# Performance work log

Measured on AMD Instinct MI355X. Metric: run time of the kernel, lower is better.

Reference implementation:

```python
import jax, jax.numpy as jnp
import numpy as np

BATCH = 4096
NUM_FEATURES = 2048
DEPTH = 4
KERNEL = 2
THRESHOLD = 0.0


def setup_inputs() -> dict:
    key = jax.random.key(0)
    keys = jax.random.split(key, 2 + 2 * DEPTH + 2)
    inp = {}
    inp['x'] = jax.random.normal(keys[0], (BATCH, NUM_FEATURES), dtype=jnp.float32)
    # Conv2d(1,1,kernel_size=2) weight (k,k) and scalar bias, PyTorch-style init scale
    fan_in = KERNEL * KERNEL
    bound = 1.0 / np.sqrt(fan_in)
    inp['conv_w'] = jax.random.uniform(keys[1], (KERNEL, KERNEL), jnp.float32, -bound, bound)
    inp['conv_b'] = jax.random.uniform(keys[2], (), jnp.float32, -bound, bound)
    # MLP hidden layers
    lb = 1.0 / np.sqrt(NUM_FEATURES)
    for i in range(DEPTH):
        inp[f'W{i}'] = jax.random.uniform(keys[3 + 2 * i], (NUM_FEATURES, NUM_FEATURES), jnp.float32, -lb, lb)
        inp[f'b{i}'] = jax.random.uniform(keys[4 + 2 * i], (NUM_FEATURES,), jnp.float32, -lb, lb)
    inp['Wh'] = jax.random.uniform(keys[3 + 2 * DEPTH], (2, NUM_FEATURES), jnp.float32, -lb, lb)
    inp['bh'] = jax.random.uniform(keys[4 + 2 * DEPTH], (2,), jnp.float32, -lb, lb)
    return inp


def reference(x, conv_w, conv_b, W0, b0, W1, b1, W2, b2, W3, b3, Wh, bh):
    # Per-feature ConvFilter on a constant k x k patch of value x_i collapses to
    # sigmoid(x_i * sum(conv_w) + conv_b - threshold)  -- one fused elementwise op.
    h = jax.nn.sigmoid(x * jnp.sum(conv_w) + conv_b - THRESHOLD)  # (B, F)
    for W, b in ((W0, b0), (W1, b1), (W2, b2), (W3, b3)):
        h = jax.nn.relu(h @ W.T + b)
    return h @ Wh.T + bh  # (B, 2)
```

## Files before the change

kernel.cpp:

```cpp
#include <hip/hip_runtime.h>
#include <math.h>

#define BATCH 4096
#define NF    2048

typedef signed char    i8;
typedef unsigned int   u32;
typedef __attribute__((ext_vector_type(4))) int   intx4;
typedef __attribute__((ext_vector_type(4))) float floatx4;

#define LBW 0.022097086912079612f
#define QMAX 32512.0f
#define AMAX_H 3.0f

__global__ __launch_bounds__(256) void prep_kernel(
    const float* __restrict__ x, const float* __restrict__ cw,
    const float* __restrict__ cb,
    const float* __restrict__ w0, const float* __restrict__ w1,
    const float* __restrict__ w2, const float* __restrict__ w3,
    i8* __restrict__ h1o, i8* __restrict__ h2o,
    i8* __restrict__ q1,  i8* __restrict__ q2)
{
    const int bid = blockIdx.x;
    if (bid < 8192) {
        const float s = cw[0] + cw[1] + cw[2] + cw[3];
        const float c = cb[0];
        const int i = bid * 256 + threadIdx.x;
        float4 v = ((const float4*)x)[i];
        float vv[4] = {v.x, v.y, v.z, v.w};
        char4 c1, c2;
        #pragma unroll
        for (int j = 0; j < 4; ++j) {
            float r = 1.0f / (1.0f + expf(-(vv[j] * s + c)));
            int X = (int)(r * QMAX + 0.5f);
            int h1 = (X + 128) >> 8;
            int h2 = X - (h1 << 8);
            ((i8*)&c1)[j] = (i8)h1;
            ((i8*)&c2)[j] = (i8)h2;
        }
        *(char4*)&h1o[(size_t)i * 4] = c1;
        *(char4*)&h2o[(size_t)i * 4] = c2;
    } else {
        const int b2    = bid - 8192;
        const int layer = b2 >> 12;
        const int i     = (b2 & 4095) * 256 + threadIdx.x;
        const float* w = (layer == 0) ? w0 : (layer == 1) ? w1
                       : (layer == 2) ? w2 : w3;
        const size_t base = (size_t)layer * (size_t)NF * NF;
        float4 v = ((const float4*)w)[i];
        float vv[4] = {v.x, v.y, v.z, v.w};
        char4 c1, c2;
        #pragma unroll
        for (int j = 0; j < 4; ++j) {
            int X = (int)floorf(vv[j] * (QMAX / LBW) + 0.5f);
            X = max(-32512, min(32512, X));
            int h1 = (X + 128) >> 8;
            int h2 = X - (h1 << 8);
            ((i8*)&c1)[j] = (i8)h1;
            ((i8*)&c2)[j] = (i8)h2;
        }
        *(char4*)&q1[base + (size_t)i * 4] = c1;
        *(char4*)&q2[base + (size_t)i * 4] = c2;
    }
}

#define BM 256
#define BN 128
#define BK 64

#define BUFSZ  49152
#define SEC_A1 0
#define SEC_A2 16384
#define SEC_B1 32768
#define SEC_B2 40960

__device__ __forceinline__ void stage16(const void* g, void* l) {
    __builtin_amdgcn_global_load_lds(
        (const __attribute__((address_space(1))) u32*)g,
        (__attribute__((address_space(3))) u32*)l, 16, 0, 0);
}

__global__ __launch_bounds__(512, 2) void gemm_i8_split(
    const i8* __restrict__ A1, const i8* __restrict__ A2,
    const i8* __restrict__ B1, const i8* __restrict__ B2,
    const float* __restrict__ bias,
    i8* __restrict__ C1, i8* __restrict__ C2,
    const float* __restrict__ Wh, const float* __restrict__ bh,
    float* __restrict__ outp,
    float combo, float outscale, int last, int M, int N, int K)
{
    extern __shared__ i8 smem[];

    const int t    = threadIdx.x;
    const int wv   = t >> 6;
    const int ln   = t & 63;
    const int quad = ln >> 4;
    const int ml   = ln & 15;
    const int wm   = wv >> 1;
    const int wn   = wv & 1;
    const int bm   = blockIdx.y * BM;
    const int bn   = blockIdx.x * BN;
    const int lnoff = ln * 16;

    int rA0 = (bm + (wv * 2 + 0) * 16 + ml) * K + quad * 16;
    int rA1 = (bm + (wv * 2 + 1) * 16 + ml) * K + quad * 16;
    int rB  = (bn +  wv * 16          + ml) * K + quad * 16;

    intx4 zero = {0, 0, 0, 0};
    intx4 acc11[4][4], accX[4][4];
    #pragma unroll
    for (int i = 0; i < 4; ++i)
        #pragma unroll
        for (int j = 0; j < 4; ++j) { acc11[i][j] = zero; accX[i][j] = zero; }

    stage16(A1 + rA0, smem + 0 * BUFSZ + SEC_A1 + (wv * 2 + 0) * 1024);
    stage16(A1 + rA1, smem + 0 * BUFSZ + SEC_A1 + (wv * 2 + 1) * 1024);
    stage16(A2 + rA0, smem + 0 * BUFSZ + SEC_A2 + (wv * 2 + 0) * 1024);
    stage16(A2 + rA1, smem + 0 * BUFSZ + SEC_A2 + (wv * 2 + 1) * 1024);
    stage16(B1 + rB,  smem + 0 * BUFSZ + SEC_B1 + wv * 1024);
    stage16(B2 + rB,  smem + 0 * BUFSZ + SEC_B2 + wv * 1024);
    rA0 += BK; rA1 += BK; rB += BK;
    stage16(A1 + rA0, smem + 1 * BUFSZ + SEC_A1 + (wv * 2 + 0) * 1024);
    stage16(A1 + rA1, smem + 1 * BUFSZ + SEC_A1 + (wv * 2 + 1) * 1024);
    stage16(A2 + rA0, smem + 1 * BUFSZ + SEC_A2 + (wv * 2 + 0) * 1024);
    stage16(A2 + rA1, smem + 1 * BUFSZ + SEC_A2 + (wv * 2 + 1) * 1024);
    stage16(B1 + rB,  smem + 1 * BUFSZ + SEC_B1 + wv * 1024);
    stage16(B2 + rB,  smem + 1 * BUFSZ + SEC_B2 + wv * 1024);
    rA0 += BK; rA1 += BK; rB += BK;
    asm volatile("s_waitcnt vmcnt(6)" ::: "memory");
    __builtin_amdgcn_s_barrier();
    asm volatile("" ::: "memory");

    int rdbase = 0;
    int wrbase = 2 * BUFSZ;

    intx4 a1f0, a1f1, a2f0, a2f1;
    intx4 b1lo0, b1lo1, b2lo0, b2lo1, b1hi0, b1hi1, b2hi0, b2hi1;

#define LDA_(SEC, c) (*(const intx4*)&smem[rdbase + (SEC) + (c) * 1024 + lnoff])
#define MFMA3(i, j, A1R, A2R, B1R, B2R) \
    acc11[i][j] = __builtin_amdgcn_mfma_i32_16x16x64_i8(A1R, B1R, acc11[i][j], 0, 0, 0); \
    accX [i][j] = __builtin_amdgcn_mfma_i32_16x16x64_i8(A1R, B2R, accX [i][j], 0, 0, 0); \
    accX [i][j] = __builtin_amdgcn_mfma_i32_16x16x64_i8(A2R, B1R, accX [i][j], 0, 0, 0);
#define FENCE_   asm volatile("" ::: "memory")
#define BARRIER_ FENCE_; __builtin_amdgcn_s_barrier(); FENCE_
#define LGKM0_   asm volatile("s_waitcnt lgkmcnt(0)" ::: "memory")

    const int NIT = K >> 6;
    #pragma unroll 1
    for (int kt = 0; kt < NIT; ++kt) {
        const int sg = (kt < NIT - 2);
        a1f0 = LDA_(SEC_A1, wm * 4 + 0);  a1f1 = LDA_(SEC_A1, wm * 4 + 1);
        a2f0 = LDA_(SEC_A2, wm * 4 + 0);  a2f1 = LDA_(SEC_A2, wm * 4 + 1);
        b1lo0 = LDA_(SEC_B1, wn * 4 + 0); b1lo1 = LDA_(SEC_B1, wn * 4 + 1);
        b2lo0 = LDA_(SEC_B2, wn * 4 + 0); b2lo1 = LDA_(SEC_B2, wn * 4 + 1);
        if (sg) {
            stage16(A1 + rA0, smem + wrbase + SEC_A1 + (wv * 2 + 0) * 1024);
            stage16(A1 + rA1, smem + wrbase + SEC_A1 + (wv * 2 + 1) * 1024);
            stage16(A2 + rA0, smem + wrbase + SEC_A2 + (wv * 2 + 0) * 1024);
            stage16(A2 + rA1, smem + wrbase + SEC_A2 + (wv * 2 + 1) * 1024);
        }
        BARRIER_; LGKM0_;
        __builtin_amdgcn_s_setprio(1);
        MFMA3(0, 0, a1f0, a2f0, b1lo0, b2lo0) MFMA3(0, 1, a1f0, a2f0, b1lo1, b2lo1)
        MFMA3(1, 0, a1f1, a2f1, b1lo0, b2lo0) MFMA3(1, 1, a1f1, a2f1, b1lo1, b2lo1)
        __builtin_amdgcn_s_setprio(0);
        BARRIER_;
        b1hi0 = LDA_(SEC_B1, wn * 4 + 2); b1hi1 = LDA_(SEC_B1, wn * 4 + 3);
        b2hi0 = LDA_(SEC_B2, wn * 4 + 2); b2hi1 = LDA_(SEC_B2, wn * 4 + 3);
        if (sg) {
            stage16(B1 + rB, smem + wrbase + SEC_B1 + wv * 1024);
            stage16(B2 + rB, smem + wrbase + SEC_B2 + wv * 1024);
            rA0 += BK; rA1 += BK; rB += BK;
        }
        BARRIER_; LGKM0_;
        __builtin_amdgcn_s_setprio(1);
        MFMA3(0, 2, a1f0, a2f0, b1hi0, b2hi0) MFMA3(0, 3, a1f0, a2f0, b1hi1, b2hi1)
        MFMA3(1, 2, a1f1, a2f1, b1hi0, b2hi0) MFMA3(1, 3, a1f1, a2f1, b1hi1, b2hi1)
        __builtin_amdgcn_s_setprio(0);
        BARRIER_;
        a1f0 = LDA_(SEC_A1, wm * 4 + 2);  a1f1 = LDA_(SEC_A1, wm * 4 + 3);
        a2f0 = LDA_(SEC_A2, wm * 4 + 2);  a2f1 = LDA_(SEC_A2, wm * 4 + 3);
        BARRIER_; LGKM0_;
        __builtin_amdgcn_s_setprio(1);
        MFMA3(2, 2, a1f0, a2f0, b1hi0, b2hi0) MFMA3(2, 3, a1f0, a2f0, b1hi1, b2hi1)
        MFMA3(3, 2, a1f1, a2f1, b1hi0, b2hi0) MFMA3(3, 3, a1f1, a2f1, b1hi1, b2hi1)
        __builtin_amdgcn_s_setprio(0);
        if (sg) { asm volatile("s_waitcnt vmcnt(6)" ::: "memory"); }
        else    { asm volatile("s_waitcnt vmcnt(0)" ::: "memory"); }
        BARRIER_;
        __builtin_amdgcn_s_setprio(1);
        MFMA3(2, 0, a1f0, a2f0, b1lo0, b2lo0) MFMA3(2, 1, a1f0, a2f0, b1lo1, b2lo1)
        MFMA3(3, 0, a1f1, a2f1, b1lo0, b2lo0) MFMA3(3, 1, a1f1, a2f1, b1lo1, b2lo1)
        __builtin_amdgcn_s_setprio(0);
        rdbase = (rdbase == 2 * BUFSZ) ? 0 : rdbase + BUFSZ;
        wrbase = (wrbase == 2 * BUFSZ) ? 0 : wrbase + BUFSZ;
    }

#undef LDA_
#undef MFMA3
#undef FENCE_
#undef BARRIER_
#undef LGKM0_

    if (!last) {
        #pragma unroll
        for (int j = 0; j < 4; ++j) {
            const int n  = bn + wn * 64 + j * 16 + ml;
            const float bv = bias[n];
            #pragma unroll
            for (int i = 0; i < 4; ++i) {
                #pragma unroll
                for (int r = 0; r < 4; ++r) {
                    const int m = bm + wm * 64 + i * 16 + quad * 4 + r;
                    float v = fmaf(65536.0f, (float)acc11[i][j][r],
                                   256.0f * (float)accX[i][j][r]) * combo + bv;
                    v = fmaxf(v, 0.0f);
                    int X = (int)(fminf(v * outscale, QMAX) + 0.5f);
                    int h1 = (X + 128) >> 8;
                    int h2 = X - (h1 << 8);
                    C1[(size_t)m * N + n] = (i8)h1;
                    C2[(size_t)m * N + n] = (i8)h2;
                }
            }
        }
    } else {
        float wh0[4], wh1[4], bv[4];
        #pragma unroll
        for (int j = 0; j < 4; ++j) {
            const int n = bn + wn * 64 + j * 16 + ml;
            bv[j]  = bias[n];
            wh0[j] = Wh[n];
            wh1[j] = Wh[NF + n];
        }
        #pragma unroll
        for (int i = 0; i < 4; ++i) {
            #pragma unroll
            for (int r = 0; r < 4; ++r) {
                float s0 = 0.0f, s1 = 0.0f;
                #pragma unroll
                for (int j = 0; j < 4; ++j) {
                    float v = fmaf(65536.0f, (float)acc11[i][j][r],
                                   256.0f * (float)accX[i][j][r]) * combo + bv[j];
                    v = fmaxf(v, 0.0f);
                    s0 = fmaf(v, wh0[j], s0);
                    s1 = fmaf(v, wh1[j], s1);
                }
                #pragma unroll
                for (int off = 8; off > 0; off >>= 1) {
                    s0 += __shfl_xor(s0, off, 64);
                    s1 += __shfl_xor(s1, off, 64);
                }
                if (ml == 0) {
                    const int m = bm + wm * 64 + i * 16 + quad * 4 + r;
                    if (bn == 0 && wn == 0) { s0 += bh[0]; s1 += bh[1]; }
                    atomicAdd(&outp[(size_t)m * 2 + 0], s0);
                    atomicAdd(&outp[(size_t)m * 2 + 1], s1);
                }
            }
        }
    }
}

__global__ __launch_bounds__(256) void act_kernel_f32(
    const float* __restrict__ x, const float* __restrict__ conv_w,
    const float* __restrict__ conv_b, float* __restrict__ h, int n4)
{
    const float s = conv_w[0] + conv_w[1] + conv_w[2] + conv_w[3];
    const float c = conv_b[0];
    int i = blockIdx.x * blockDim.x + threadIdx.x;
    if (i < n4) {
        float4 v = ((const float4*)x)[i];
        float4 r;
        r.x = 1.0f / (1.0f + expf(-(v.x * s + c)));
        r.y = 1.0f / (1.0f + expf(-(v.y * s + c)));
        r.z = 1.0f / (1.0f + expf(-(v.z * s + c)));
        r.w = 1.0f / (1.0f + expf(-(v.w * s + c)));
        ((float4*)h)[i] = r;
    }
}

#define FBM 128
#define FBN 128
#define FBK 16
#define FPAD 4

__global__ __launch_bounds__(256) void gemm_bias_relu_f32(
    const float* __restrict__ A, const float* __restrict__ W,
    const float* __restrict__ bias, float* __restrict__ C,
    int M, int N, int K, int do_relu)
{
    __shared__ float As[FBK][FBM + FPAD];
    __shared__ float Bs[FBK][FBN + FPAD];
    const int t  = threadIdx.x;
    const int bm = blockIdx.y * FBM;
    const int bn = blockIdx.x * FBN;
    const int tn = (t & 15) * 8;
    const int tm = (t >> 4) * 8;
    const int r0 = t >> 2;
    const int kv = (t & 3) << 2;
    float acc[8][8] = {};
    for (int k0 = 0; k0 < K; k0 += FBK) {
        #pragma unroll
        for (int half = 0; half < 2; ++half) {
            const int row = r0 + half * 64;
            float4 av = *(const float4*)&A[(size_t)(bm + row) * K + k0 + kv];
            As[kv + 0][row] = av.x; As[kv + 1][row] = av.y;
            As[kv + 2][row] = av.z; As[kv + 3][row] = av.w;
            float4 bv = *(const float4*)&W[(size_t)(bn + row) * K + k0 + kv];
            Bs[kv + 0][row] = bv.x; Bs[kv + 1][row] = bv.y;
            Bs[kv + 2][row] = bv.z; Bs[kv + 3][row] = bv.w;
        }
        __syncthreads();
        #pragma unroll
        for (int kk = 0; kk < FBK; ++kk) {
            float a[8], b[8];
            *(float4*)&a[0] = *(const float4*)&As[kk][tm];
            *(float4*)&a[4] = *(const float4*)&As[kk][tm + 4];
            *(float4*)&b[0] = *(const float4*)&Bs[kk][tn];
            *(float4*)&b[4] = *(const float4*)&Bs[kk][tn + 4];
            #pragma unroll
            for (int i = 0; i < 8; ++i)
                #pragma unroll
                for (int j = 0; j < 8; ++j)
                    acc[i][j] = fmaf(a[i], b[j], acc[i][j]);
        }
        __syncthreads();
    }
    #pragma unroll
    for (int i = 0; i < 8; ++i) {
        const int row = bm + tm + i;
        #pragma unroll
        for (int j = 0; j < 8; j += 4) {
            float4 v;
            v.x = acc[i][j + 0] + bias[bn + tn + j + 0];
            v.y = acc[i][j + 1] + bias[bn + tn + j + 1];
            v.z = acc[i][j + 2] + bias[bn + tn + j + 2];
            v.w = acc[i][j + 3] + bias[bn + tn + j + 3];
            if (do_relu) {
                v.x = fmaxf(v.x, 0.0f); v.y = fmaxf(v.y, 0.0f);
                v.z = fmaxf(v.z, 0.0f); v.w = fmaxf(v.w, 0.0f);
            }
            *(float4*)&C[(size_t)row * N + bn + tn + j] = v;
        }
    }
}

__global__ __launch_bounds__(256) void head_kernel_f32(
    const float* __restrict__ h, const float* __restrict__ Wh,
    const float* __restrict__ bh, float* __restrict__ out)
{
    const int wave = threadIdx.x >> 6;
    const int lane = threadIdx.x & 63;
    const int row  = blockIdx.x * 4 + wave;
    const float* hr = h + (size_t)row * NF;
    float acc0 = 0.0f, acc1 = 0.0f;
    for (int k = lane * 4; k < NF; k += 256) {
        float4 v  = *(const float4*)&hr[k];
        float4 w0 = *(const float4*)&Wh[k];
        float4 w1 = *(const float4*)&Wh[NF + k];
        acc0 += v.x * w0.x + v.y * w0.y + v.z * w0.z + v.w * w0.w;
        acc1 += v.x * w1.x + v.y * w1.y + v.z * w1.z + v.w * w1.w;
    }
    #pragma unroll
    for (int off = 32; off > 0; off >>= 1) {
        acc0 += __shfl_down(acc0, off, 64);
        acc1 += __shfl_down(acc1, off, 64);
    }
    if (lane == 0) {
        out[row * 2 + 0] = acc0 + bh[0];
        out[row * 2 + 1] = acc1 + bh[1];
    }
}

extern "C" void kernel_launch(void* const* d_in, const int* in_sizes, int n_in,
                              void* d_out, int out_size, void* d_ws, size_t ws_size,
                              hipStream_t stream)
{
    const float* x      = (const float*)d_in[0];
    const float* conv_w = (const float*)d_in[1];
    const float* conv_b = (const float*)d_in[2];
    const float* Ws[4]  = {(const float*)d_in[3], (const float*)d_in[5],
                           (const float*)d_in[7], (const float*)d_in[9]};
    const float* bs[4]  = {(const float*)d_in[4], (const float*)d_in[6],
                           (const float*)d_in[8], (const float*)d_in[10]};
    const float* Wh     = (const float*)d_in[11];
    const float* bh     = (const float*)d_in[12];
    float* out = (float*)d_out;

    const size_t AE = (size_t)BATCH * NF;
    const size_t WE = (size_t)NF * NF;
    const size_t need_i8 = 4 * AE + 8 * WE;

    const int n4 = (BATCH * NF) / 4;

    if (ws_size >= need_i8) {
        static int attr_done = 0;
        if (!attr_done) {
            (void)hipFuncSetAttribute(
                reinterpret_cast<const void*>(gemm_i8_split),
                hipFuncAttributeMaxDynamicSharedMemorySize, 3 * BUFSZ);
            attr_done = 1;
        }

        i8* base = (i8*)d_ws;
        i8* a01 = base;
        i8* a02 = a01 + AE;
        i8* a11 = a02 + AE;
        i8* a12 = a11 + AE;
        i8* wq1 = a12 + AE;
        i8* wq2 = wq1 + 4 * WE;

        hipMemsetAsync(out, 0, (size_t)out_size * sizeof(float), stream);

        prep_kernel<<<8192 + 16384, 256, 0, stream>>>(
            x, conv_w, conv_b, Ws[0], Ws[1], Ws[2], Ws[3],
            a01, a02, wq1, wq2);

        const float sW = LBW / QMAX;
        const float outscale = QMAX / AMAX_H;
        dim3 grid(NF / BN, BATCH / BM);

        i8 *in1 = a01, *in2 = a02, *o1 = a11, *o2 = a12;
        for (int l = 0; l < 4; ++l) {
            const float sA = ((l == 0) ? 1.0f : AMAX_H) / QMAX;
            gemm_i8_split<<<grid, 512, 3 * BUFSZ, stream>>>(
                in1, in2, wq1 + (size_t)l * WE, wq2 + (size_t)l * WE,
                bs[l], o1, o2, Wh, bh, out,
                sA * sW, outscale, (l == 3) ? 1 : 0, BATCH, NF, NF);
            i8* t1 = in1; i8* t2 = in2;
            in1 = o1; in2 = o2; o1 = t1; o2 = t2;
        }
    } else {
        float* ws0 = (float*)d_ws;
        float* ws1 = ws0 + AE;
        act_kernel_f32<<<(n4 + 255) / 256, 256, 0, stream>>>(x, conv_w, conv_b, ws0, n4);
        dim3 fgrid(NF / FBN, BATCH / FBM);
        gemm_bias_relu_f32<<<fgrid, 256, 0, stream>>>(ws0, Ws[0], bs[0], ws1, BATCH, NF, NF, 1);
        gemm_bias_relu_f32<<<fgrid, 256, 0, stream>>>(ws1, Ws[1], bs[1], ws0, BATCH, NF, NF, 1);
        gemm_bias_relu_f32<<<fgrid, 256, 0, stream>>>(ws0, Ws[2], bs[2], ws1, BATCH, NF, NF, 1);
        gemm_bias_relu_f32<<<fgrid, 256, 0, stream>>>(ws1, Ws[3], bs[3], ws0, BATCH, NF, NF, 1);
        head_kernel_f32<<<BATCH / 4, 256, 0, stream>>>(ws0, Wh, bh, out);
    }
}
```

Baseline: 364.1 us.

## Replace ping-pong phased MFMA schedule with a single load-then-compute loop body

Removes the four-phase barrier/setprio schedule that interleaved LDS fragment loads, global stages and MFMA clusters. Each iteration now issues all global stages, loads all A/B fragments into registers at once, runs all 48 MFMAs, then waits and hits one barrier. This cuts barrier count and simplifies scheduling, but gives up the fine-grained overlap between waves and raises register pressure from holding 16 fragments at once.

```diff
diff --git a/kernel.cpp b/kernel.cpp
--- a/kernel.cpp
+++ b/kernel.cpp
@@ -134,74 +134,47 @@
     int rdbase = 0;
     int wrbase = 2 * BUFSZ;
 
-    intx4 a1f0, a1f1, a2f0, a2f1;
-    intx4 b1lo0, b1lo1, b2lo0, b2lo1, b1hi0, b1hi1, b2hi0, b2hi1;
-
 #define LDA_(SEC, c) (*(const intx4*)&smem[rdbase + (SEC) + (c) * 1024 + lnoff])
-#define MFMA3(i, j, A1R, A2R, B1R, B2R) \
-    acc11[i][j] = __builtin_amdgcn_mfma_i32_16x16x64_i8(A1R, B1R, acc11[i][j], 0, 0, 0); \
-    accX [i][j] = __builtin_amdgcn_mfma_i32_16x16x64_i8(A1R, B2R, accX [i][j], 0, 0, 0); \
-    accX [i][j] = __builtin_amdgcn_mfma_i32_16x16x64_i8(A2R, B1R, accX [i][j], 0, 0, 0);
-#define FENCE_   asm volatile("" ::: "memory")
-#define BARRIER_ FENCE_; __builtin_amdgcn_s_barrier(); FENCE_
-#define LGKM0_   asm volatile("s_waitcnt lgkmcnt(0)" ::: "memory")
 
     const int NIT = K >> 6;
     #pragma unroll 1
     for (int kt = 0; kt < NIT; ++kt) {
         const int sg = (kt < NIT - 2);
-        a1f0 = LDA_(SEC_A1, wm * 4 + 0);  a1f1 = LDA_(SEC_A1, wm * 4 + 1);
-        a2f0 = LDA_(SEC_A2, wm * 4 + 0);  a2f1 = LDA_(SEC_A2, wm * 4 + 1);
-        b1lo0 = LDA_(SEC_B1, wn * 4 + 0); b1lo1 = LDA_(SEC_B1, wn * 4 + 1);
-        b2lo0 = LDA_(SEC_B2, wn * 4 + 0); b2lo1 = LDA_(SEC_B2, wn * 4 + 1);
         if (sg) {
             stage16(A1 + rA0, smem + wrbase + SEC_A1 + (wv * 2 + 0) * 1024);
             stage16(A1 + rA1, smem + wrbase + SEC_A1 + (wv * 2 + 1) * 1024);
             stage16(A2 + rA0, smem + wrbase + SEC_A2 + (wv * 2 + 0) * 1024);
             stage16(A2 + rA1, smem + wrbase + SEC_A2 + (wv * 2 + 1) * 1024);
-        }
-        BARRIER_; LGKM0_;
-        __builtin_amdgcn_s_setprio(1);
-        MFMA3(0, 0, a1f0, a2f0, b1lo0, b2lo0) MFMA3(0, 1, a1f0, a2f0, b1lo1, b2lo1)
-        MFMA3(1, 0, a1f1, a2f1, b1lo0, b2lo0) MFMA3(1, 1, a1f1, a2f1, b1lo1, b2lo1)
-        __builtin_amdgcn_s_setprio(0);
-        BARRIER_;
-        b1hi0 = LDA_(SEC_B1, wn * 4 + 2); b1hi1 = LDA_(SEC_B1, wn * 4 + 3);
-        b2hi0 = LDA_(SEC_B2, wn * 4 + 2); b2hi1 = LDA_(SEC_B2, wn * 4 + 3);
-        if (sg) {
-            stage16(B1 + rB, smem + wrbase + SEC_B1 + wv * 1024);
-            stage16(B2 + rB, smem + wrbase + SEC_B2 + wv * 1024);
+            stage16(B1 + rB,  smem + wrbase + SEC_B1 + wv * 1024);
+            stage16(B2 + rB,  smem + wrbase + SEC_B2 + wv * 1024);
             rA0 += BK; rA1 += BK; rB += BK;
         }
-        BARRIER_; LGKM0_;
-        __builtin_amdgcn_s_setprio(1);
-        MFMA3(0, 2, a1f0, a2f0, b1hi0, b2hi0) MFMA3(0, 3, a1f0, a2f0, b1hi1, b2hi1)
-        MFMA3(1, 2, a1f1, a2f1, b1hi0, b2hi0) MFMA3(1, 3, a1f1, a2f1, b1hi1, b2hi1)
-        __builtin_amdgcn_s_setprio(0);
-        BARRIER_;
-        a1f0 = LDA_(SEC_A1, wm * 4 + 2);  a1f1 = LDA_(SEC_A1, wm * 4 + 3);
-        a2f0 = LDA_(SEC_A2, wm * 4 + 2);  a2f1 = LDA_(SEC_A2, wm * 4 + 3);
-        BARRIER_; LGKM0_;
-        __builtin_amdgcn_s_setprio(1);
-        MFMA3(2, 2, a1f0, a2f0, b1hi0, b2hi0) MFMA3(2, 3, a1f0, a2f0, b1hi1, b2hi1)
-        MFMA3(3, 2, a1f1, a2f1, b1hi0, b2hi0) MFMA3(3, 3, a1f1, a2f1, b1hi1, b2hi1)
-        __builtin_amdgcn_s_setprio(0);
+        intx4 a1[4], a2[4], b1[4], b2[4];
+        #pragma unroll
+        for (int i = 0; i < 4; ++i) {
+            a1[i] = LDA_(SEC_A1, wm * 4 + i);
+            a2[i] = LDA_(SEC_A2, wm * 4 + i);
+            b1[i] = LDA_(SEC_B1, wn * 4 + i);
+            b2[i] = LDA_(SEC_B2, wn * 4 + i);
+        }
+        #pragma unroll
+        for (int j = 0; j < 4; ++j) {
+            #pragma unroll
+            for (int i = 0; i < 4; ++i) {
+                acc11[i][j] = __builtin_amdgcn_mfma_i32_16x16x64_i8(a1[i], b1[j], acc11[i][j], 0, 0, 0);
+                accX [i][j] = __builtin_amdgcn_mfma_i32_16x16x64_i8(a1[i], b2[j], accX [i][j], 0, 0, 0);
+                accX [i][j] = __builtin_amdgcn_mfma_i32_16x16x64_i8(a2[i], b1[j], accX [i][j], 0, 0, 0);
+            }
+        }
         if (sg) { asm volatile("s_waitcnt vmcnt(6)" ::: "memory"); }
         else    { asm volatile("s_waitcnt vmcnt(0)" ::: "memory"); }
-        BARRIER_;
-        __builtin_amdgcn_s_setprio(1);
-        MFMA3(2, 0, a1f0, a2f0, b1lo0, b2lo0) MFMA3(2, 1, a1f0, a2f0, b1lo1, b2lo1)
-        MFMA3(3, 0, a1f1, a2f1, b1lo0, b2lo0) MFMA3(3, 1, a1f1, a2f1, b1lo1, b2lo1)
-        __builtin_amdgcn_s_setprio(0);
+        __builtin_amdgcn_s_barrier();
+        asm volatile("" ::: "memory");
         rdbase = (rdbase == 2 * BUFSZ) ? 0 : rdbase + BUFSZ;
         wrbase = (wrbase == 2 * BUFSZ) ? 0 : wrbase + BUFSZ;
     }
 
 #undef LDA_
-#undef MFMA3
-#undef FENCE_
-#undef BARRIER_
-#undef LGKM0_
 
     if (!last) {
         #pragma unroll
```

Result: no change. 363.8 us (-0.1%).
